# Kernel optimization log

Measured on AMD Instinct MI355X. Metric: run time of the kernel, lower is better.

Reference implementation:

```python
import jax, jax.numpy as jnp
import numpy as np

X_WEIGHT = 1.0
Y_WEIGHT = 1.0


def setup_inputs() -> dict:
    key = jax.random.key(0)
    k1, k2 = jax.random.split(key)
    B, C, H, W = 32, 8, 256, 256
    inp = jax.random.normal(k1, (B, C, H, W), dtype=jnp.float32)
    tgt = jax.random.uniform(k2, (B, C, H, W), dtype=jnp.float32)
    return {"input": inp, "target": tgt}


def reference(input, target):
    B, C, H, W = input.shape
    # coordinate maps: x[j] = (j+1 - W/2)/W, y[p] = (p+1 - H/2)/H  (tanh half-range)
    xs = (jnp.arange(W, dtype=jnp.float32) + 1.0 - W / 2.0) / W  # [W]
    ys = (jnp.arange(H, dtype=jnp.float32) + 1.0 - H / 2.0) / H  # [H]

    # DSNT: softmax over each flattened heatmap, then coordinate expectation
    p = jax.nn.softmax(input.reshape(B, C, H * W), axis=-1).reshape(B, C, H, W)
    pred_x = jnp.einsum('bchw,w->bc', p, xs)  # [B, C]
    pred_y = jnp.einsum('bchw,h->bc', p, ys)  # [B, C]

    # ground truth via argmax of target heatmap, converted to same coord range
    idx = jnp.argmax(target.reshape(B, C, H * W), axis=-1)  # [B, C] int
    true_x = ((idx % W).astype(jnp.float32) + 1.0 - W / 2.0) / W
    true_y = ((idx // W).astype(jnp.float32) + 1.0 - H / 2.0) / H

    # per-heatmap MSE over the 2-vector (x, y), each weighted
    dx = pred_x * X_WEIGHT - true_x * X_WEIGHT
    dy = pred_y * Y_WEIGHT - true_y * Y_WEIGHT
    mse = 0.5 * (dx * dx + dy * dy)  # [B, C]

    # original sums over all B*C heatmaps, then divides by B (i+1 == batch size)
    return jnp.sum(mse) / B
```

## Files before the change

kernel.cpp:

```cpp
#include <hip/hip_runtime.h>
#include <math.h>

#define HW 65536
#define F4_PER_MAP 16384
#define NMAPS 256
#define THREADS 256
#define CHUNKS 2
#define F4_PER_BLOCK 8192
#define DEPTH 16
#define ROUNDS 2

#define SHIFT_M 8.0f

__global__ __launch_bounds__(THREADS, 4) void dsnt_pass1(const float* __restrict__ input,
                                                         const float* __restrict__ target,
                                                         float4* __restrict__ wsA,
                                                         float2* __restrict__ wsB) {
    const int b    = blockIdx.x;
    const int role = b & 1;
    const int id   = b >> 1;
    const int tid  = threadIdx.x;
    const int wave = tid >> 6, lane = tid & 63;

    const float LOG2E  = 1.4426950408889634f;
    const float INV256 = 1.0f / 256.0f;
    const float NSH    = -SHIFT_M * LOG2E;

    __shared__ float red0[4], red1[4], red2[4];
    __shared__ int   red3[4];

    if (role == 0) {
        const float4* p = (const float4*)input + (size_t)id * F4_PER_BLOCK;

        float4 buf[DEPTH];
#pragma unroll
        for (int k = 0; k < DEPTH; ++k) buf[k] = p[tid + k * THREADS];

        float s0 = 0.f, s1 = 0.f, sx0 = 0.f, sx1 = 0.f, sy0 = 0.f, sy1 = 0.f;

#pragma unroll
        for (int j = 0; j < ROUNDS; ++j) {
#pragma unroll
            for (int k = 0; k < DEPTH; ++k) {
                float4 vv = buf[k];
                if (j + 1 < ROUNDS)
                    buf[k] = p[tid + ((j + 1) * DEPTH + k) * THREADS];

                int Q  = id * F4_PER_BLOCK + (j * DEPTH + k) * THREADS + tid;
                int lq = Q & (F4_PER_MAP - 1);
                int h  = lq >> 6;
                int w0 = (lq & 63) << 2;
                float cy  = (float)(h  - 127) * INV256;
                float cx0 = (float)(w0 - 127) * INV256;

                float e0 = __builtin_exp2f(fmaf(vv.x, LOG2E, NSH));
                float e1 = __builtin_exp2f(fmaf(vv.y, LOG2E, NSH));
                float e2 = __builtin_exp2f(fmaf(vv.z, LOG2E, NSH));
                float e3 = __builtin_exp2f(fmaf(vv.w, LOG2E, NSH));
                float esum  = (e0 + e1) + (e2 + e3);
                float exsum = fmaf(e0, cx0,
                              fmaf(e1, cx0 + INV256,
                              fmaf(e2, cx0 + 2.f * INV256,
                                   e3 * (cx0 + 3.f * INV256))));
                if (k & 1) { s1 += esum; sx1 += exsum; sy1 = fmaf(esum, cy, sy1); }
                else       { s0 += esum; sx0 += exsum; sy0 = fmaf(esum, cy, sy0); }
            }
        }
        float s = s0 + s1, sx = sx0 + sx1, sy = sy0 + sy1;

#pragma unroll
        for (int k = 1; k < 64; k <<= 1) {
            s  += __shfl_xor(s,  k, 64);
            sx += __shfl_xor(sx, k, 64);
            sy += __shfl_xor(sy, k, 64);
        }
        if (lane == 0) { red0[wave] = s; red1[wave] = sx; red2[wave] = sy; }
        __syncthreads();
        if (tid == 0) {
            s  = (red0[0] + red0[1]) + (red0[2] + red0[3]);
            sx = (red1[0] + red1[1]) + (red1[2] + red1[3]);
            sy = (red2[0] + red2[1]) + (red2[2] + red2[3]);
            wsA[id] = make_float4(s, sx, sy, 0.f);
        }
    } else {
        const float4* p = (const float4*)target + (size_t)id * F4_PER_BLOCK;

        float4 buf[DEPTH];
#pragma unroll
        for (int k = 0; k < DEPTH; ++k) buf[k] = p[tid + k * THREADS];

        float tv = -INFINITY;
        int   ti = 0x7fffffff;

#pragma unroll
        for (int j = 0; j < ROUNDS; ++j) {
#pragma unroll
            for (int k = 0; k < DEPTH; ++k) {
                float4 tt = buf[k];
                if (j + 1 < ROUNDS)
                    buf[k] = p[tid + ((j + 1) * DEPTH + k) * THREADS];

                int Q  = id * F4_PER_BLOCK + (j * DEPTH + k) * THREADS + tid;
                int lq = Q & (F4_PER_MAP - 1);
                int j0 = lq << 2;
                if (tt.x > tv) { tv = tt.x; ti = j0;     }
                if (tt.y > tv) { tv = tt.y; ti = j0 + 1; }
                if (tt.z > tv) { tv = tt.z; ti = j0 + 2; }
                if (tt.w > tv) { tv = tt.w; ti = j0 + 3; }
            }
        }
#pragma unroll
        for (int k = 1; k < 64; k <<= 1) {
            float otv = __shfl_xor(tv, k, 64);
            int   oti = __shfl_xor(ti, k, 64);
            bool take = (otv > tv) || (otv == tv && oti < ti);
            tv = take ? otv : tv;
            ti = take ? oti : ti;
        }
        if (lane == 0) { red0[wave] = tv; red3[wave] = ti; }
        __syncthreads();
        if (tid == 0) {
            tv = red0[0]; ti = red3[0];
            for (int i = 1; i < 4; ++i) {
                float otv = red0[i]; int oti = red3[i];
                if (otv > tv || (otv == tv && oti < ti)) { tv = otv; ti = oti; }
            }
            wsB[id] = make_float2(tv, __int_as_float(ti));
        }
    }
}

__global__ __launch_bounds__(NMAPS) void dsnt_pass2(const float4* __restrict__ wsA,
                                                    const float2* __restrict__ wsB,
                                                    float* __restrict__ out) {
    const int t = threadIdx.x;
    const float INV256 = 1.0f / 256.0f;

    float s = 0.f, sx = 0.f, sy = 0.f;
    float tv = -INFINITY;
    int   ti = 0x7fffffff;
#pragma unroll
    for (int c = 0; c < CHUNKS; ++c) {
        float4 a = wsA[t * CHUNKS + c];
        s += a.x; sx += a.y; sy += a.z;
        float2 bb = wsB[t * CHUNKS + c];
        int oti = __float_as_int(bb.y);
        if (bb.x > tv || (bb.x == tv && oti < ti)) { tv = bb.x; ti = oti; }
    }
    float px = sx / s, py = sy / s;
    float tx = (float)((ti & 255) - 127) * INV256;
    float ty = (float)((ti >> 8)  - 127) * INV256;
    float dx = px - tx, dy = py - ty;
    float loss = 0.5f * (dx * dx + dy * dy);

#pragma unroll
    for (int k = 32; k > 0; k >>= 1) loss += __shfl_down(loss, k, 64);
    __shared__ float partial[4];
    int wave = t >> 6, lane = t & 63;
    if (lane == 0) partial[wave] = loss;
    __syncthreads();
    if (t == 0) {
        float total = (partial[0] + partial[1]) + (partial[2] + partial[3]);
        out[0] = total * (1.0f / 32.0f);
    }
}

extern "C" void kernel_launch(void* const* d_in, const int* in_sizes, int n_in,
                              void* d_out, int out_size, void* d_ws, size_t ws_size,
                              hipStream_t stream) {
    const float* input  = (const float*)d_in[0];
    const float* target = (const float*)d_in[1];
    float4* wsA = (float4*)d_ws;
    float2* wsB = (float2*)((char*)d_ws + 512 * sizeof(float4));
    float*  out = (float*)d_out;

    dsnt_pass1<<<2 * 512, THREADS, 0, stream>>>(input, target, wsA, wsB);
    dsnt_pass2<<<1, NMAPS, 0, stream>>>(wsA, wsB, out);
}
```

Measured before the change: 146.7 us.

## Stream heatmaps through per-wave LDS ring via async global_load_lds

Measured after the change: 142.6 us. -2.8%, faster.

```diff
diff --git a/kernel.cpp b/kernel.cpp
--- a/kernel.cpp
+++ b/kernel.cpp
@@ -7,15 +7,23 @@
 #define THREADS 256
 #define CHUNKS 2
 #define F4_PER_BLOCK 8192
-#define DEPTH 16
-#define ROUNDS 2
+#define F4_PER_WAVE 2048
+#define SLOTS 8
+#define ITERS 32
 
 #define SHIFT_M 8.0f
 
-__global__ __launch_bounds__(THREADS, 4) void dsnt_pass1(const float* __restrict__ input,
-                                                         const float* __restrict__ target,
-                                                         float4* __restrict__ wsA,
-                                                         float2* __restrict__ wsB) {
+__device__ __forceinline__ void gload_lds16(const float4* gsrc, void* lds_dst) {
+    __builtin_amdgcn_global_load_lds(
+        (const __attribute__((address_space(1))) void*)gsrc,
+        (__attribute__((address_space(3))) void*)lds_dst,
+        16, 0, 0);
+}
+
+__global__ __launch_bounds__(THREADS) void dsnt_pass1(const float* __restrict__ input,
+                                                      const float* __restrict__ target,
+                                                      float4* __restrict__ wsA,
+                                                      float2* __restrict__ wsB) {
     const int b    = blockIdx.x;
     const int role = b & 1;
     const int id   = b >> 1;
@@ -26,45 +34,46 @@
     const float INV256 = 1.0f / 256.0f;
     const float NSH    = -SHIFT_M * LOG2E;
 
+    __shared__ float4 ring[4 * SLOTS * 64];
+    float4* wave_ring = &ring[wave * (SLOTS * 64)];
+
     __shared__ float red0[4], red1[4], red2[4];
     __shared__ int   red3[4];
 
-    if (role == 0) {
-        const float4* p = (const float4*)input + (size_t)id * F4_PER_BLOCK;
-
-        float4 buf[DEPTH];
-#pragma unroll
-        for (int k = 0; k < DEPTH; ++k) buf[k] = p[tid + k * THREADS];
-
-        float s0 = 0.f, s1 = 0.f, sx0 = 0.f, sx1 = 0.f, sy0 = 0.f, sy1 = 0.f;
+    const float4* src = (role == 0) ? (const float4*)input : (const float4*)target;
+    const float4* p = src + (size_t)id * F4_PER_BLOCK + wave * F4_PER_WAVE + lane;
 
 #pragma unroll
-        for (int j = 0; j < ROUNDS; ++j) {
-#pragma unroll
-            for (int k = 0; k < DEPTH; ++k) {
-                float4 vv = buf[k];
-                if (j + 1 < ROUNDS)
-                    buf[k] = p[tid + ((j + 1) * DEPTH + k) * THREADS];
+    for (int s = 0; s < SLOTS; ++s)
+        gload_lds16(p + s * 64, &wave_ring[s * 64]);
 
-                int Q  = id * F4_PER_BLOCK + (j * DEPTH + k) * THREADS + tid;
-                int lq = Q & (F4_PER_MAP - 1);
-                int h  = lq >> 6;
-                int w0 = (lq & 63) << 2;
-                float cy  = (float)(h  - 127) * INV256;
-                float cx0 = (float)(w0 - 127) * INV256;
+    if (role == 0) {
+        float s0 = 0.f, s1 = 0.f, sx0 = 0.f, sx1 = 0.f, sy0 = 0.f, sy1 = 0.f;
+#pragma unroll 8
+        for (int it = 0; it < ITERS; ++it) {
+            int slot = it & (SLOTS - 1);
+            float4 vv = wave_ring[slot * 64 + lane];
+            if (it + SLOTS < ITERS)
+                gload_lds16(p + (it + SLOTS) * 64, &wave_ring[slot * 64]);
 
-                float e0 = __builtin_exp2f(fmaf(vv.x, LOG2E, NSH));
-                float e1 = __builtin_exp2f(fmaf(vv.y, LOG2E, NSH));
-                float e2 = __builtin_exp2f(fmaf(vv.z, LOG2E, NSH));
-                float e3 = __builtin_exp2f(fmaf(vv.w, LOG2E, NSH));
-                float esum  = (e0 + e1) + (e2 + e3);
-                float exsum = fmaf(e0, cx0,
-                              fmaf(e1, cx0 + INV256,
-                              fmaf(e2, cx0 + 2.f * INV256,
-                                   e3 * (cx0 + 3.f * INV256))));
-                if (k & 1) { s1 += esum; sx1 += exsum; sy1 = fmaf(esum, cy, sy1); }
-                else       { s0 += esum; sx0 += exsum; sy0 = fmaf(esum, cy, sy0); }
-            }
+            int F  = id * F4_PER_BLOCK + wave * F4_PER_WAVE + it * 64 + lane;
+            int lq = F & (F4_PER_MAP - 1);
+            int h  = lq >> 6;
+            int w0 = (lq & 63) << 2;
+            float cy  = (float)(h  - 127) * INV256;
+            float cx0 = (float)(w0 - 127) * INV256;
+
+            float e0 = __builtin_exp2f(fmaf(vv.x, LOG2E, NSH));
+            float e1 = __builtin_exp2f(fmaf(vv.y, LOG2E, NSH));
+            float e2 = __builtin_exp2f(fmaf(vv.z, LOG2E, NSH));
+            float e3 = __builtin_exp2f(fmaf(vv.w, LOG2E, NSH));
+            float esum  = (e0 + e1) + (e2 + e3);
+            float exsum = fmaf(e0, cx0,
+                          fmaf(e1, cx0 + INV256,
+                          fmaf(e2, cx0 + 2.f * INV256,
+                               e3 * (cx0 + 3.f * INV256))));
+            if (it & 1) { s1 += esum; sx1 += exsum; sy1 = fmaf(esum, cy, sy1); }
+            else        { s0 += esum; sx0 += exsum; sy0 = fmaf(esum, cy, sy0); }
         }
         float s = s0 + s1, sx = sx0 + sx1, sy = sy0 + sy1;
 
@@ -83,31 +92,21 @@
             wsA[id] = make_float4(s, sx, sy, 0.f);
         }
     } else {
-        const float4* p = (const float4*)target + (size_t)id * F4_PER_BLOCK;
-
-        float4 buf[DEPTH];
-#pragma unroll
-        for (int k = 0; k < DEPTH; ++k) buf[k] = p[tid + k * THREADS];
-
         float tv = -INFINITY;
         int   ti = 0x7fffffff;
+#pragma unroll 8
+        for (int it = 0; it < ITERS; ++it) {
+            int slot = it & (SLOTS - 1);
+            float4 tt = wave_ring[slot * 64 + lane];
+            if (it + SLOTS < ITERS)
+                gload_lds16(p + (it + SLOTS) * 64, &wave_ring[slot * 64]);
 
-#pragma unroll
-        for (int j = 0; j < ROUNDS; ++j) {
-#pragma unroll
-            for (int k = 0; k < DEPTH; ++k) {
-                float4 tt = buf[k];
-                if (j + 1 < ROUNDS)
-                    buf[k] = p[tid + ((j + 1) * DEPTH + k) * THREADS];
-
-                int Q  = id * F4_PER_BLOCK + (j * DEPTH + k) * THREADS + tid;
-                int lq = Q & (F4_PER_MAP - 1);
-                int j0 = lq << 2;
-                if (tt.x > tv) { tv = tt.x; ti = j0;     }
-                if (tt.y > tv) { tv = tt.y; ti = j0 + 1; }
-                if (tt.z > tv) { tv = tt.z; ti = j0 + 2; }
-                if (tt.w > tv) { tv = tt.w; ti = j0 + 3; }
-            }
+            int F  = id * F4_PER_BLOCK + wave * F4_PER_WAVE + it * 64 + lane;
+            int j0 = (F & (F4_PER_MAP - 1)) << 2;
+            if (tt.x > tv) { tv = tt.x; ti = j0;     }
+            if (tt.y > tv) { tv = tt.y; ti = j0 + 1; }
+            if (tt.z > tv) { tv = tt.z; ti = j0 + 2; }
+            if (tt.w > tv) { tv = tt.w; ti = j0 + 3; }
         }
 #pragma unroll
         for (int k = 1; k < 64; k <<= 1) {
```
